# Kernel optimization log

Hardware: AMD Instinct MI355X
Metric: run time of the kernel (lower is better)

## Reference

```python
import jax, jax.numpy as jnp
import numpy as np
from jax import lax

DIM = 96
B, H, W = 4, 256, 256


def setup_inputs() -> dict:
    key = jax.random.key(0)
    ks = jax.random.split(key, 20)
    f = lambda k, s, scale=0.05: (jax.random.normal(k, s, dtype=jnp.float32) * scale)
    d = DIM
    return {
        "x": jax.random.normal(ks[0], (B, d, H, W), dtype=jnp.float32),
        "prompt": jax.random.normal(ks[1], (B, d), dtype=jnp.float32),
        "scale_weights": jax.random.uniform(ks[2], (B, 3), dtype=jnp.float32),
        "ln_w": jnp.ones((d,), jnp.float32),
        "ln_b": jnp.zeros((d,), jnp.float32),
        "e0_pw_w": f(ks[3], (d, d)),       # expert0 pointwise 1x1: [out, in]
        "e0_pw_b": f(ks[4], (d,)),
        "e0_dw_w": f(ks[5], (d, 1, 3, 3)),  # depthwise 3x3
        "e0_dw_b": f(ks[6], (d,)),
        "e1_dw_w": f(ks[7], (d, 1, 3, 3)),  # depthwise 3x3, dilation 2
        "e1_dw_b": f(ks[8], (d,)),
        "e2_dw_w": f(ks[9], (d, 1, 5, 5)),  # depthwise 5x5, dilation 3
        "e2_dw_b": f(ks[10], (d,)),
        "proj_w": f(ks[11], (d, d)),
        "proj_b": f(ks[12], (d,)),
        "ffn1_w": f(ks[13], (2 * d, d)),
        "ffn1_b": f(ks[14], (2 * d,)),
        "ffn2_w": f(ks[15], (d, 2 * d)),
        "ffn2_b": f(ks[16], (d,)),
    }


def _conv1x1(x, w, b):
    # x: [B,C,H,W], w: [O,C]
    return jnp.einsum('bchw,oc->bohw', x, w) + b[None, :, None, None]


def _dwconv(x, w, b, dilation, pad):
    # depthwise conv, w: [C,1,k,k]
    c = x.shape[1]
    y = lax.conv_general_dilated(
        x, w, window_strides=(1, 1),
        padding=[(pad, pad), (pad, pad)],
        rhs_dilation=(dilation, dilation),
        feature_group_count=c,
        dimension_numbers=('NCHW', 'OIHW', 'NCHW'))
    return y + b[None, :, None, None]


def _layernorm_c(x, w, b, eps=1e-6):
    # LayerNorm over channel dim of NCHW (torch permutes to NHWC, norms last dim)
    mu = jnp.mean(x, axis=1, keepdims=True)
    var = jnp.mean((x - mu) ** 2, axis=1, keepdims=True)
    xn = (x - mu) * lax.rsqrt(var + eps)
    return xn * w[None, :, None, None] + b[None, :, None, None]


def reference(x, prompt, scale_weights, ln_w, ln_b,
              e0_pw_w, e0_pw_b, e0_dw_w, e0_dw_b,
              e1_dw_w, e1_dw_b, e2_dw_w, e2_dw_b,
              proj_w, proj_b, ffn1_w, ffn1_b, ffn2_w, ffn2_b):
    shortcut = x
    xn = _layernorm_c(x, ln_w, ln_b)

    # Three receptive-field experts (all run densely, soft-weighted)
    e0 = _dwconv(_conv1x1(xn, e0_pw_w, e0_pw_b), e0_dw_w, e0_dw_b, dilation=1, pad=1)
    e1 = _dwconv(xn, e1_dw_w, e1_dw_b, dilation=2, pad=2)
    e2 = _dwconv(xn, e2_dw_w, e2_dw_b, dilation=3, pad=6)

    w = scale_weights  # [B,3]
    x_adaptive = (w[:, 0, None, None, None] * e0
                  + w[:, 1, None, None, None] * e1
                  + w[:, 2, None, None, None] * e2)
    x_adaptive = x_adaptive * (1.0 + prompt[:, :, None, None])

    x1 = shortcut + _conv1x1(x_adaptive, proj_w, proj_b)
    h = jax.nn.gelu(_conv1x1(x1, ffn1_w, ffn1_b), approximate=False)
    out = x1 + _conv1x1(h, ffn2_w, ffn2_b)
    return out
```

## Files before the change

### kernel.cpp

```cpp
#include <hip/hip_runtime.h>
#include <hip/hip_bf16.h>

typedef __hip_bfloat16 bf16;
typedef __attribute__((ext_vector_type(8))) __bf16 bf16x8;
typedef __attribute__((ext_vector_type(4))) float  f32x4;

#define HW   65536
#define WID  256
#define CC   96
#define NB   4
static const size_t S_ELEMS = (size_t)NB * CC * HW;

__device__ __forceinline__ float lo2f(unsigned u) { unsigned x = u << 16;        return __builtin_bit_cast(float, x); }
__device__ __forceinline__ float hi2f(unsigned u) { unsigned x = u & 0xffff0000u; return __builtin_bit_cast(float, x); }
__device__ __forceinline__ unsigned short f2bu(float f) {
    return __builtin_bit_cast(unsigned short, __float2bfloat16(f));
}

__device__ __forceinline__ float gelu_erf(float v) {
    float z  = fabsf(v) * 0.70710678118654752f;
    float t  = __builtin_amdgcn_rcpf(1.f + 0.3275911f * z);
    float poly = t * (0.254829592f + t * (-0.284496736f + t * (1.421413741f
               + t * (-1.453152027f + t * 1.061405429f))));
    float erfz = 1.f - poly * __expf(-z * z);
    float erfv = copysignf(erfz, v);
    return 0.5f * v * (1.f + erfv);
}

__global__ __launch_bounds__(256) void ln_kernel(
    const float* __restrict__ x, const float* __restrict__ lw,
    const float* __restrict__ lb, bf16* __restrict__ y)
{
    int t  = blockIdx.x * 256 + threadIdx.x;
    int b  = t >> 15;
    int hw = (t & 32767) * 2;
    size_t base = (size_t)b * CC * HW + hw;

    float s0 = 0.f, s1 = 0.f, q0 = 0.f, q1 = 0.f;
    for (int c = 0; c < CC; ++c) {
        float2 v = *reinterpret_cast<const float2*>(&x[base + (size_t)c * HW]);
        s0 += v.x; s1 += v.y; q0 += v.x * v.x; q1 += v.y * v.y;
    }
    float mu0 = s0 * (1.f / 96.f), mu1 = s1 * (1.f / 96.f);
    float rs0 = rsqrtf(q0 * (1.f / 96.f) - mu0 * mu0 + 1e-6f);
    float rs1 = rsqrtf(q1 * (1.f / 96.f) - mu1 * mu1 + 1e-6f);

    for (int c = 0; c < CC; ++c) {
        float2 v = *reinterpret_cast<const float2*>(&x[base + (size_t)c * HW]);
        float g = lw[c], be = lb[c];
        bf16 o[2];
        o[0] = __float2bfloat16((v.x - mu0) * rs0 * g + be);
        o[1] = __float2bfloat16((v.y - mu1) * rs1 * g + be);
        *reinterpret_cast<uint*>(&y[base + (size_t)c * HW]) = *reinterpret_cast<uint*>(o);
    }
}

__device__ __forceinline__ int swzo(int row, int col, int width) {
    return (row * width + col) ^ ((((row & 7) ^ ((row >> 3) & 7)) << 3));
}

template <typename TI, typename TOT, int CIN, int COUT, bool GELU, bool HASRES>
__global__ __launch_bounds__(256) void conv1x1_mfma(
    const TI* __restrict__ in, const float* __restrict__ wgt,
    const float* __restrict__ bias, const float* __restrict__ resid,
    TOT* __restrict__ out)
{
    constexpr int KSPLIT = CIN / 96;
    constexpr int OSPLIT = COUT / 96;
    constexpr int MT     = 6;
    static_assert(CIN == KSPLIT * 96 && COUT == OSPLIT * 96, "96-multiples only");

    __shared__ unsigned short s_w[96 * 96];
    __shared__ unsigned short s_x[128 * 96];
    __shared__ float          s_b[COUT];

    const int tid  = threadIdx.x;
    const int lane = tid & 63;
    const int wave = tid >> 6;
    const int q    = lane >> 4;
    const int n    = lane & 15;

    const int pos0 = blockIdx.x * 128;
    const int b    = pos0 >> 16;
    const int hw0  = pos0 & 65535;

    for (int k = tid; k < COUT; k += 256) s_b[k] = bias[k];

    const TI* inb = in + (size_t)b * CIN * HW;
    const int pl0 = wave * 32 + n;
    const int pl1 = pl0 + 16;

#pragma unroll
    for (int os = 0; os < OSPLIT; ++os) {
        f32x4 acc[MT][2];
#pragma unroll
        for (int mt = 0; mt < MT; ++mt) {
            acc[mt][0] = {0.f, 0.f, 0.f, 0.f};
            acc[mt][1] = {0.f, 0.f, 0.f, 0.f};
        }

#pragma unroll
        for (int ks = 0; ks < KSPLIT; ++ks) {
            for (int k = tid; k < 96 * 24; k += 256) {
                int o = k / 24, c4 = (k - o * 24) * 4;
                float4 w4 = *reinterpret_cast<const float4*>(
                    &wgt[(size_t)(os * 96 + o) * CIN + ks * 96 + c4]);
                ushort4 pk = make_ushort4(f2bu(w4.x), f2bu(w4.y), f2bu(w4.z), f2bu(w4.w));
                *reinterpret_cast<ushort4*>(&s_w[swzo(o, c4, 96)]) = pk;
            }
            if (KSPLIT > 1 || os == 0) {
                for (int idx = tid; idx < 48 * 16; idx += 256) {
                    const int cp = idx >> 4;
                    const int pb = idx & 15;
                    const TI* gp = inb + (size_t)(ks * 96 + 2 * cp) * HW + hw0 + pb * 8;
                    unsigned short ua[8], ub[8];
                    if constexpr (__is_same(TI, float)) {
                        float4 a0 = *reinterpret_cast<const float4*>(gp);
                        float4 a1 = *reinterpret_cast<const float4*>(gp + 4);
                        float4 b0 = *reinterpret_cast<const float4*>(gp + HW);
                        float4 b1 = *reinterpret_cast<const float4*>(gp + HW + 4);
                        ua[0]=f2bu(a0.x); ua[1]=f2bu(a0.y); ua[2]=f2bu(a0.z); ua[3]=f2bu(a0.w);
                        ua[4]=f2bu(a1.x); ua[5]=f2bu(a1.y); ua[6]=f2bu(a1.z); ua[7]=f2bu(a1.w);
                        ub[0]=f2bu(b0.x); ub[1]=f2bu(b0.y); ub[2]=f2bu(b0.z); ub[3]=f2bu(b0.w);
                        ub[4]=f2bu(b1.x); ub[5]=f2bu(b1.y); ub[6]=f2bu(b1.z); ub[7]=f2bu(b1.w);
                    } else {
                        *reinterpret_cast<uint4*>(ua) = *reinterpret_cast<const uint4*>(gp);
                        *reinterpret_cast<uint4*>(ub) = *reinterpret_cast<const uint4*>(gp + HW);
                    }
#pragma unroll
                    for (int i = 0; i < 8; ++i) {
                        uint d = (uint)ua[i] | ((uint)ub[i] << 16);
                        *reinterpret_cast<uint*>(&s_x[swzo(pb * 8 + i, 2 * cp, 96)]) = d;
                    }
                }
            }
            __syncthreads();

#pragma unroll
            for (int kt = 0; kt < 3; ++kt) {
                const int col = kt * 32 + q * 8;
                union { unsigned short u[8]; bf16x8 v; } bf0, bf1;
                *reinterpret_cast<uint4*>(bf0.u) =
                    *reinterpret_cast<const uint4*>(&s_x[swzo(pl0, col, 96)]);
                *reinterpret_cast<uint4*>(bf1.u) =
                    *reinterpret_cast<const uint4*>(&s_x[swzo(pl1, col, 96)]);
#pragma unroll
                for (int mt = 0; mt < MT; ++mt) {
                    union { unsigned short u[8]; bf16x8 v; } fa;
                    *reinterpret_cast<uint4*>(fa.u) =
                        *reinterpret_cast<const uint4*>(&s_w[swzo(mt * 16 + n, col, 96)]);
                    acc[mt][0] = __builtin_amdgcn_mfma_f32_16x16x32_bf16(fa.v, bf0.v, acc[mt][0], 0, 0, 0);
                    acc[mt][1] = __builtin_amdgcn_mfma_f32_16x16x32_bf16(fa.v, bf1.v, acc[mt][1], 0, 0, 0);
                }
            }
            if (os + 1 < OSPLIT || ks + 1 < KSPLIT)
                __syncthreads();
        }

        const int p0 = hw0 + pl0;
        const int p1 = hw0 + pl1;
        const size_t obase = (size_t)b * COUT * HW;
#pragma unroll
        for (int mt = 0; mt < MT; ++mt) {
#pragma unroll
            for (int nt = 0; nt < 2; ++nt) {
                const int p = (nt == 0) ? p0 : p1;
#pragma unroll
                for (int r = 0; r < 4; ++r) {
                    const int o = os * 96 + mt * 16 + q * 4 + r;
                    float v = acc[mt][nt][r] + s_b[o];
                    if constexpr (GELU) v = gelu_erf(v);
                    const size_t idx = obase + (size_t)o * HW + p;
                    if constexpr (HASRES) v += resid[idx];
                    if constexpr (__is_same(TOT, float)) out[idx] = v;
                    else                                 out[idx] = __float2bfloat16(v);
                }
            }
        }
    }
}

__global__ __launch_bounds__(256) void ffn_fused(
    const bf16* __restrict__ xa, const float* __restrict__ x,
    const float* __restrict__ pw, const float* __restrict__ pb,
    const float* __restrict__ w1, const float* __restrict__ b1,
    const float* __restrict__ w2, const float* __restrict__ b2,
    float* __restrict__ out)
{
    constexpr int HP = 104;
    __shared__ unsigned short s_w[96 * 96];
    __shared__ unsigned short s_x1[128 * HP];
    __shared__ unsigned short s_hx[128 * HP];
    __shared__ float          s_bias[384];

    const int tid  = threadIdx.x;
    const int lane = tid & 63;
    const int wave = tid >> 6;
    const int q    = lane >> 4;
    const int n    = lane & 15;

    const int pos0 = blockIdx.x * 128;
    const int b    = pos0 >> 16;
    const int hw0  = pos0 & 65535;
    const int pl0  = wave * 32 + n;
    const int pl1  = pl0 + 16;

    auto stage_w = [&](const float* W, int row0, int col0, int rstride) {
        for (int k = tid; k < 96 * 24; k += 256) {
            int o = k / 24, c4 = (k - o * 24) * 4;
            float4 w4 = *reinterpret_cast<const float4*>(
                &W[(size_t)(row0 + o) * rstride + col0 + c4]);
            ushort4 pk = make_ushort4(f2bu(w4.x), f2bu(w4.y), f2bu(w4.z), f2bu(w4.w));
            *reinterpret_cast<ushort4*>(&s_w[swzo(o, c4, 96)]) = pk;
        }
    };
    auto gemm_swz = [&](f32x4 (&acc)[6][2]) {
#pragma unroll
        for (int kt = 0; kt < 3; ++kt) {
            const int col = kt * 32 + q * 8;
            union { unsigned short u[8]; bf16x8 v; } bf0, bf1;
            *reinterpret_cast<uint4*>(bf0.u) =
                *reinterpret_cast<const uint4*>(&s_hx[swzo(pl0, col, 96)]);
            *reinterpret_cast<uint4*>(bf1.u) =
                *reinterpret_cast<const uint4*>(&s_hx[swzo(pl1, col, 96)]);
#pragma unroll
            for (int mt = 0; mt < 6; ++mt) {
                union { unsigned short u[8]; bf16x8 v; } fa;
                *reinterpret_cast<uint4*>(fa.u) =
                    *reinterpret_cast<const uint4*>(&s_w[swzo(mt * 16 + n, col, 96)]);
                acc[mt][0] = __builtin_amdgcn_mfma_f32_16x16x32_bf16(fa.v, bf0.v, acc[mt][0], 0, 0, 0);
                acc[mt][1] = __builtin_amdgcn_mfma_f32_16x16x32_bf16(fa.v, bf1.v, acc[mt][1], 0, 0, 0);
            }
        }
    };
    auto gemm_lin = [&](const unsigned short* B, f32x4 (&acc)[6][2]) {
#pragma unroll
        for (int kt = 0; kt < 3; ++kt) {
            const int col = kt * 32 + q * 8;
            union { unsigned short u[8]; bf16x8 v; } bf0, bf1;
            *reinterpret_cast<uint4*>(bf0.u) =
                *reinterpret_cast<const uint4*>(&B[pl0 * HP + col]);
            *reinterpret_cast<uint4*>(bf1.u) =
                *reinterpret_cast<const uint4*>(&B[pl1 * HP + col]);
#pragma unroll
            for (int mt = 0; mt < 6; ++mt) {
                union { unsigned short u[8]; bf16x8 v; } fa;
                *reinterpret_cast<uint4*>(fa.u) =
                    *reinterpret_cast<const uint4*>(&s_w[swzo(mt * 16 + n, col, 96)]);
                acc[mt][0] = __builtin_amdgcn_mfma_f32_16x16x32_bf16(fa.v, bf0.v, acc[mt][0], 0, 0, 0);
                acc[mt][1] = __builtin_amdgcn_mfma_f32_16x16x32_bf16(fa.v, bf1.v, acc[mt][1], 0, 0, 0);
            }
        }
    };
    auto st4 = [&](unsigned short* dst, int elem, float v0, float v1, float v2, float v3) {
        union { unsigned short u[4]; uint2 d; } t;
        t.u[0] = f2bu(v0); t.u[1] = f2bu(v1); t.u[2] = f2bu(v2); t.u[3] = f2bu(v3);
        *reinterpret_cast<uint2*>(&dst[elem]) = t.d;
    };

    {
        const bf16* inb = xa + (size_t)b * 96 * HW;
        for (int idx = tid; idx < 48 * 16; idx += 256) {
            const int cp = idx >> 4, pbk = idx & 15;
            const bf16* gp = inb + (size_t)(2 * cp) * HW + hw0 + pbk * 8;
            unsigned short ua[8], ub[8];
            *reinterpret_cast<uint4*>(ua) = *reinterpret_cast<const uint4*>(gp);
            *reinterpret_cast<uint4*>(ub) = *reinterpret_cast<const uint4*>(gp + HW);
#pragma unroll
            for (int i = 0; i < 8; ++i) {
                uint d = (uint)ua[i] | ((uint)ub[i] << 16);
                *reinterpret_cast<uint*>(&s_hx[swzo(pbk * 8 + i, 2 * cp, 96)]) = d;
            }
        }
    }
    stage_w(pw, 0, 0, 96);
    if (tid < 96)  s_bias[tid]       = pb[tid];
    if (tid < 192) s_bias[96 + tid]  = b1[tid];
    if (tid < 96)  s_bias[288 + tid] = b2[tid];
    __syncthreads();

    float xr[6][2][4];
    {
        const size_t xbase = (size_t)b * 96 * HW;
#pragma unroll
        for (int mt = 0; mt < 6; ++mt)
#pragma unroll
            for (int nt = 0; nt < 2; ++nt) {
                const int p = hw0 + (nt ? pl1 : pl0);
#pragma unroll
                for (int r = 0; r < 4; ++r)
                    xr[mt][nt][r] = x[xbase + (size_t)(mt * 16 + q * 4 + r) * HW + p];
            }
    }
    f32x4 accp[6][2];
#pragma unroll
    for (int mt = 0; mt < 6; ++mt) { accp[mt][0] = {0,0,0,0}; accp[mt][1] = {0,0,0,0}; }
    gemm_swz(accp);

    float x1f[6][2][4];
#pragma unroll
    for (int mt = 0; mt < 6; ++mt)
#pragma unroll
        for (int nt = 0; nt < 2; ++nt) {
            const int p = nt ? pl1 : pl0;
#pragma unroll
            for (int r = 0; r < 4; ++r)
                x1f[mt][nt][r] = accp[mt][nt][r] + s_bias[mt * 16 + q * 4 + r] + xr[mt][nt][r];
            st4(s_x1, p * HP + mt * 16 + q * 4,
                x1f[mt][nt][0], x1f[mt][nt][1], x1f[mt][nt][2], x1f[mt][nt][3]);
        }
    __syncthreads();

    stage_w(w1, 0, 0, 96);
    __syncthreads();
    f32x4 acc1[6][2];
#pragma unroll
    for (int mt = 0; mt < 6; ++mt) { acc1[mt][0] = {0,0,0,0}; acc1[mt][1] = {0,0,0,0}; }
    gemm_lin(s_x1, acc1);
#pragma unroll
    for (int mt = 0; mt < 6; ++mt)
#pragma unroll
        for (int nt = 0; nt < 2; ++nt) {
            const int p = nt ? pl1 : pl0;
            float v0 = gelu_erf(acc1[mt][nt][0] + s_bias[96 + mt * 16 + q * 4 + 0]);
            float v1 = gelu_erf(acc1[mt][nt][1] + s_bias[96 + mt * 16 + q * 4 + 1]);
            float v2 = gelu_erf(acc1[mt][nt][2] + s_bias[96 + mt * 16 + q * 4 + 2]);
            float v3 = gelu_erf(acc1[mt][nt][3] + s_bias[96 + mt * 16 + q * 4 + 3]);
            st4(s_hx, p * HP + mt * 16 + q * 4, v0, v1, v2, v3);
        }
    __syncthreads();

    stage_w(w1, 96, 0, 96);
    __syncthreads();
    f32x4 acc1b[6][2];
#pragma unroll
    for (int mt = 0; mt < 6; ++mt) { acc1b[mt][0] = {0,0,0,0}; acc1b[mt][1] = {0,0,0,0}; }
    gemm_lin(s_x1, acc1b);
    __syncthreads();

    stage_w(w2, 0, 0, 192);
    __syncthreads();
    f32x4 acc2[6][2];
#pragma unroll
    for (int mt = 0; mt < 6; ++mt) { acc2[mt][0] = {0,0,0,0}; acc2[mt][1] = {0,0,0,0}; }
    gemm_lin(s_hx, acc2);
    __syncthreads();

    stage_w(w2, 0, 96, 192);
#pragma unroll
    for (int mt = 0; mt < 6; ++mt)
#pragma unroll
        for (int nt = 0; nt < 2; ++nt) {
            const int p = nt ? pl1 : pl0;
            float v0 = gelu_erf(acc1b[mt][nt][0] + s_bias[192 + mt * 16 + q * 4 + 0]);
            float v1 = gelu_erf(acc1b[mt][nt][1] + s_bias[192 + mt * 16 + q * 4 + 1]);
            float v2 = gelu_erf(acc1b[mt][nt][2] + s_bias[192 + mt * 16 + q * 4 + 2]);
            float v3 = gelu_erf(acc1b[mt][nt][3] + s_bias[192 + mt * 16 + q * 4 + 3]);
            st4(s_hx, p * HP + mt * 16 + q * 4, v0, v1, v2, v3);
        }
    __syncthreads();
    gemm_lin(s_hx, acc2);

    const size_t obase = (size_t)b * 96 * HW;
#pragma unroll
    for (int mt = 0; mt < 6; ++mt)
#pragma unroll
        for (int nt = 0; nt < 2; ++nt) {
            const int p = hw0 + (nt ? pl1 : pl0);
#pragma unroll
            for (int r = 0; r < 4; ++r) {
                const int o = mt * 16 + q * 4 + r;
                out[obase + (size_t)o * HW + p] =
                    x1f[mt][nt][r] + acc2[mt][nt][r] + s_bias[288 + o];
            }
        }
}

#define XR     20
#define XPITCH 22
#define TPITCH 10
#define XCOLS  268
#define TCOLS  258

__global__ __launch_bounds__(256) void experts_kernel(
    const bf16* __restrict__ xn, const bf16* __restrict__ t0,
    const float* __restrict__ w0, const float* __restrict__ b0,
    const float* __restrict__ w1, const float* __restrict__ b1,
    const float* __restrict__ w2, const float* __restrict__ b2,
    const float* __restrict__ sw, const float* __restrict__ prompt,
    bf16* __restrict__ xa)
{
    __shared__ alignas(16) unsigned short sxT[XCOLS * XPITCH];
    __shared__ alignas(16) unsigned short stT[TCOLS * TPITCH];

    const int tid  = threadIdx.x;
    const int lane = tid & 63;
    const int wave = tid >> 6;
    const int bid = blockIdx.x;
    const int h0  = (bid & 31) * 8;
    const int bc  = bid >> 5;
    const int b   = bc / 96;
    const int c   = bc - b * 96;
    const size_t pbase = (size_t)bc * HW;

    const bf16* xp = xn + pbase;
    const bf16* tp = t0 + pbase;
    uint* sx32 = reinterpret_cast<uint*>(sxT);
    uint* st32 = reinterpret_cast<uint*>(stT);

    if (tid < 132) {
        int cc = tid / 11, d = tid - cc * 11;
        int col = (cc < 6) ? cc : 256 + cc;
        sx32[col * 11 + d] = 0u;
    } else if (tid < 142) {
        int i = tid - 132;
        int col = (i < 5) ? 0 : 257;
        int d   = (i < 5) ? i : i - 5;
        st32[col * 5 + d] = 0u;
    }

    {
        const int rp = (lane >> 2) & 7;
        const int ch = 8 * wave + (lane & 3) + ((lane >> 5) << 2);
        const int gh0 = h0 - 6 + 2 * rp, gh1 = gh0 + 1;
        union { uint4 q; unsigned short u[8]; } a, bb;
        a.q  = ((unsigned)gh0 < 256u) ? *reinterpret_cast<const uint4*>(xp + gh0 * WID + ch * 8)
                                      : make_uint4(0u, 0u, 0u, 0u);
        bb.q = ((unsigned)gh1 < 256u) ? *reinterpret_cast<const uint4*>(xp + gh1 * WID + ch * 8)
                                      : make_uint4(0u, 0u, 0u, 0u);
        const int base = 11 * (6 + 8 * ch) + rp;
#pragma unroll
        for (int j = 0; j < 8; ++j)
            sx32[base + 11 * j] = (uint)a.u[j] | ((uint)bb.u[j] << 16);
    }
    if (wave == 2) {
        const int rp = 8 + ((lane >> 2) & 1);
        const int ch = (lane & 3) + (((lane >> 3) & 7) << 2);
        const int gh0 = h0 - 6 + 2 * rp, gh1 = gh0 + 1;
        union { uint4 q; unsigned short u[8]; } a, bb;
        a.q  = ((unsigned)gh0 < 256u) ? *reinterpret_cast<const uint4*>(xp + gh0 * WID + ch * 8)
                                      : make_uint4(0u, 0u, 0u, 0u);
        bb.q = ((unsigned)gh1 < 256u) ? *reinterpret_cast<const uint4*>(xp + gh1 * WID + ch * 8)
                                      : make_uint4(0u, 0u, 0u, 0u);
        const int base = 11 * (6 + 8 * ch) + rp;
#pragma unroll
        for (int j = 0; j < 8; ++j)
            sx32[base + 11 * j] = (uint)a.u[j] | ((uint)bb.u[j] << 16);
    }
    if (wave < 2) {
        const int rp = (lane >> 3) & 3;
        const int ch = 16 * wave + (lane & 7) + ((lane >> 5) << 3);
        const int gh0 = h0 - 1 + 2 * rp, gh1 = gh0 + 1;
        union { uint4 q; unsigned short u[8]; } a, bb;
        a.q  = ((unsigned)gh0 < 256u) ? *reinterpret_cast<const uint4*>(tp + gh0 * WID + ch * 8)
                                      : make_uint4(0u, 0u, 0u, 0u);
        bb.q = ((unsigned)gh1 < 256u) ? *reinterpret_cast<const uint4*>(tp + gh1 * WID + ch * 8)
                                      : make_uint4(0u, 0u, 0u, 0u);
        const int base = 5 * (1 + 8 * ch) + rp;
#pragma unroll
        for (int j = 0; j < 8; ++j)
            st32[base + 5 * j] = (uint)a.u[j] | ((uint)bb.u[j] << 16);
    }
    if (wave == 3 && lane < 32) {
        const int rp = 4;
        const int ch = lane;
        const int gh0 = h0 - 1 + 2 * rp, gh1 = gh0 + 1;
        union { uint4 q; unsigned short u[8]; } a, bb;
        a.q  = ((unsigned)gh0 < 256u) ? *reinterpret_cast<const uint4*>(tp + gh0 * WID + ch * 8)
                                      : make_uint4(0u, 0u, 0u, 0u);
        bb.q = ((unsigned)gh1 < 256u) ? *reinterpret_cast<const uint4*>(tp + gh1 * WID + ch * 8)
                                      : make_uint4(0u, 0u, 0u, 0u);
        const int base = 5 * (1 + 8 * ch) + rp;
#pragma unroll
        for (int j = 0; j < 8; ++j)
            st32[base + 5 * j] = (uint)a.u[j] | ((uint)bb.u[j] << 16);
    }

    float wk0[9], wk1[9], wk2[25];
#pragma unroll
    for (int i = 0; i < 9; ++i)  wk0[i] = w0[c * 9 + i];
#pragma unroll
    for (int i = 0; i < 9; ++i)  wk1[i] = w1[c * 9 + i];
#pragma unroll
    for (int i = 0; i < 25; ++i) wk2[i] = w2[c * 25 + i];
    const float bb0 = b0[c], bb1 = b1[c], bb2 = b2[c];
    const float s0 = sw[b * 3 + 0], s1 = sw[b * 3 + 1], s2 = sw[b * 3 + 2];
    const float pr = 1.f + prompt[b * 96 + c];

    __syncthreads();

    const int w = tid;
    float acc0[8], acc1[8], acc2[8];
#pragma unroll
    for (int r = 0; r < 8; ++r) { acc0[r] = bb0; acc1[r] = bb1; acc2[r] = bb2; }

    const unsigned short* bx = &sxT[w * XPITCH];
    const unsigned short* bt = &stT[w * TPITCH];

#pragma unroll
    for (int kw = 0; kw < 5; ++kw) {
        float cv[20];
#pragma unroll
        for (int j = 0; j < 10; ++j) {
            unsigned u = *reinterpret_cast<const unsigned*>(&bx[kw * 3 * XPITCH + 2 * j]);
            cv[2 * j]     = lo2f(u);
            cv[2 * j + 1] = hi2f(u);
        }
#pragma unroll
        for (int kh = 0; kh < 5; ++kh) {
            const float wv = wk2[kh * 5 + kw];
#pragma unroll
            for (int r = 0; r < 8; ++r) acc2[r] += wv * cv[r + 3 * kh];
        }
        if (kw == 2) {
#pragma unroll
            for (int kh = 0; kh < 3; ++kh) {
                const float wv = wk1[kh * 3 + 1];
#pragma unroll
                for (int r = 0; r < 8; ++r) acc1[r] += wv * cv[r + 2 * kh + 4];
            }
        }
    }
#pragma unroll
    for (int kwh = 0; kwh < 2; ++kwh) {
        const int kw = kwh * 2;
        float cv[12];
#pragma unroll
        for (int j = 0; j < 6; ++j) {
            unsigned u = *reinterpret_cast<const unsigned*>(&bx[(4 + 2 * kw) * XPITCH + 4 + 2 * j]);
            cv[2 * j]     = lo2f(u);
            cv[2 * j + 1] = hi2f(u);
        }
#pragma unroll
        for (int kh = 0; kh < 3; ++kh) {
            const float wv = wk1[kh * 3 + kw];
#pragma unroll
            for (int r = 0; r < 8; ++r) acc1[r] += wv * cv[r + 2 * kh];
        }
    }
#pragma unroll
    for (int kw = 0; kw < 3; ++kw) {
        float cv[10];
#pragma unroll
        for (int j = 0; j < 5; ++j) {
            unsigned u = *reinterpret_cast<const unsigned*>(&bt[kw * TPITCH + 2 * j]);
            cv[2 * j]     = lo2f(u);
            cv[2 * j + 1] = hi2f(u);
        }
#pragma unroll
        for (int kh = 0; kh < 3; ++kh) {
            const float wv = wk0[kh * 3 + kw];
#pragma unroll
            for (int r = 0; r < 8; ++r) acc0[r] += wv * cv[r + kh];
        }
    }

    bf16* op = xa + pbase + (size_t)h0 * WID + w;
#pragma unroll
    for (int r = 0; r < 8; ++r) {
        float v = (s0 * acc0[r] + s1 * acc1[r] + s2 * acc2[r]) * pr;
        op[r * WID] = __float2bfloat16(v);
    }
}

extern "C" void kernel_launch(void* const* d_in, const int* in_sizes, int n_in,
                              void* d_out, int out_size, void* d_ws, size_t ws_size,
                              hipStream_t stream)
{
    const float* x       = (const float*)d_in[0];
    const float* prompt  = (const float*)d_in[1];
    const float* sw      = (const float*)d_in[2];
    const float* ln_w    = (const float*)d_in[3];
    const float* ln_b    = (const float*)d_in[4];
    const float* e0_pw_w = (const float*)d_in[5];
    const float* e0_pw_b = (const float*)d_in[6];
    const float* e0_dw_w = (const float*)d_in[7];
    const float* e0_dw_b = (const float*)d_in[8];
    const float* e1_dw_w = (const float*)d_in[9];
    const float* e1_dw_b = (const float*)d_in[10];
    const float* e2_dw_w = (const float*)d_in[11];
    const float* e2_dw_b = (const float*)d_in[12];
    const float* proj_w  = (const float*)d_in[13];
    const float* proj_b  = (const float*)d_in[14];
    const float* ffn1_w  = (const float*)d_in[15];
    const float* ffn1_b  = (const float*)d_in[16];
    const float* ffn2_w  = (const float*)d_in[17];
    const float* ffn2_b  = (const float*)d_in[18];

    float* out = (float*)d_out;
    bf16*  ws  = (bf16*)d_ws;
    bf16*  A   = ws;
    bf16*  Bt  = ws + S_ELEMS;
    bf16*  Cx  = ws + 2 * S_ELEMS;

    ln_kernel<<<512, 256, 0, stream>>>(x, ln_w, ln_b, A);
    conv1x1_mfma<bf16, bf16, 96, 96, false, false>
        <<<2048, 256, 0, stream>>>(A, e0_pw_w, e0_pw_b, nullptr, Bt);
    experts_kernel<<<12288, 256, 0, stream>>>(A, Bt, e0_dw_w, e0_dw_b, e1_dw_w, e1_dw_b,
                                              e2_dw_w, e2_dw_b, sw, prompt, Cx);
    ffn_fused<<<2048, 256, 0, stream>>>(Cx, x, proj_w, proj_b,
                                        ffn1_w, ffn1_b, ffn2_w, ffn2_b, out);
}
```

Measured before the change: 495.4 us.

## Restructure FFN kernel to 512 threads with register-prefetched weight staging

The fused proj/FFN kernel now runs 8 waves per block, each handling 16 positions instead of 32, which halves per-thread accumulator and residual register arrays. Weight tiles for the next GEMM are prefetched into registers (WLOAD) while the current GEMM runs and written to shared memory afterwards (WWRITE), hiding global weight-load latency. The x1/hidden buffers switch from padded linear layout to the swizzled layout used elsewhere. The cost is less MFMA reuse of each A fragment per wave and more barrier participants per block.

After: 491.9 us. No clear change (-0.7%).

```diff
diff --git a/kernel.cpp b/kernel.cpp
--- a/kernel.cpp
+++ b/kernel.cpp
@@ -180,87 +180,79 @@
     }
 }
 
-__global__ __launch_bounds__(256) void ffn_fused(
+__global__ __launch_bounds__(512, 4) void ffn_fused(
     const bf16* __restrict__ xa, const float* __restrict__ x,
     const float* __restrict__ pw, const float* __restrict__ pb,
     const float* __restrict__ w1, const float* __restrict__ b1,
     const float* __restrict__ w2, const float* __restrict__ b2,
     float* __restrict__ out)
 {
-    constexpr int HP = 104;
     __shared__ unsigned short s_w[96 * 96];
-    __shared__ unsigned short s_x1[128 * HP];
-    __shared__ unsigned short s_hx[128 * HP];
+    __shared__ unsigned short s_x1[128 * 96];
+    __shared__ unsigned short s_hx[128 * 96];
     __shared__ float          s_bias[384];
 
     const int tid  = threadIdx.x;
     const int lane = tid & 63;
-    const int wave = tid >> 6;
+    const int w8   = tid >> 6;
     const int q    = lane >> 4;
     const int n    = lane & 15;
 
     const int pos0 = blockIdx.x * 128;
     const int b    = pos0 >> 16;
     const int hw0  = pos0 & 65535;
-    const int pl0  = wave * 32 + n;
-    const int pl1  = pl0 + 16;
-
-    auto stage_w = [&](const float* W, int row0, int col0, int rstride) {
-        for (int k = tid; k < 96 * 24; k += 256) {
-            int o = k / 24, c4 = (k - o * 24) * 4;
-            float4 w4 = *reinterpret_cast<const float4*>(
-                &W[(size_t)(row0 + o) * rstride + col0 + c4]);
-            ushort4 pk = make_ushort4(f2bu(w4.x), f2bu(w4.y), f2bu(w4.z), f2bu(w4.w));
-            *reinterpret_cast<ushort4*>(&s_w[swzo(o, c4, 96)]) = pk;
+    const int pl   = w8 * 16 + n;
+    const int p    = hw0 + pl;
+
+    float4 wr[5];
+    auto WLOAD = [&](const float* W, int row0, int col0, int rs) {
+#pragma unroll
+        for (int i = 0; i < 5; ++i) {
+            const int idx = tid + i * 512;
+            if (i < 4 || tid < 256) {
+                const int o = idx / 24, c4 = (idx - o * 24) * 4;
+                wr[i] = *reinterpret_cast<const float4*>(
+                    &W[(size_t)(row0 + o) * rs + col0 + c4]);
+            }
         }
     };
-    auto gemm_swz = [&](f32x4 (&acc)[6][2]) {
+    auto WWRITE = [&]() {
+#pragma unroll
+        for (int i = 0; i < 5; ++i) {
+            const int idx = tid + i * 512;
+            if (i < 4 || tid < 256) {
+                const int o = idx / 24, c4 = (idx - o * 24) * 4;
+                ushort4 pk = make_ushort4(f2bu(wr[i].x), f2bu(wr[i].y),
+                                          f2bu(wr[i].z), f2bu(wr[i].w));
+                *reinterpret_cast<ushort4*>(&s_w[swzo(o, c4, 96)]) = pk;
+            }
+        }
+    };
+    auto GEMM = [&](const unsigned short* B, f32x4 (&acc)[6]) {
 #pragma unroll
         for (int kt = 0; kt < 3; ++kt) {
             const int col = kt * 32 + q * 8;
-            union { unsigned short u[8]; bf16x8 v; } bf0, bf1;
-            *reinterpret_cast<uint4*>(bf0.u) =
-                *reinterpret_cast<const uint4*>(&s_hx[swzo(pl0, col, 96)]);
-            *reinterpret_cast<uint4*>(bf1.u) =
-                *reinterpret_cast<const uint4*>(&s_hx[swzo(pl1, col, 96)]);
+            union { unsigned short u[8]; bf16x8 v; } bf;
+            *reinterpret_cast<uint4*>(bf.u) =
+                *reinterpret_cast<const uint4*>(&B[swzo(pl, col, 96)]);
 #pragma unroll
             for (int mt = 0; mt < 6; ++mt) {
                 union { unsigned short u[8]; bf16x8 v; } fa;
                 *reinterpret_cast<uint4*>(fa.u) =
                     *reinterpret_cast<const uint4*>(&s_w[swzo(mt * 16 + n, col, 96)]);
-                acc[mt][0] = __builtin_amdgcn_mfma_f32_16x16x32_bf16(fa.v, bf0.v, acc[mt][0], 0, 0, 0);
-                acc[mt][1] = __builtin_amdgcn_mfma_f32_16x16x32_bf16(fa.v, bf1.v, acc[mt][1], 0, 0, 0);
+                acc[mt] = __builtin_amdgcn_mfma_f32_16x16x32_bf16(fa.v, bf.v, acc[mt], 0, 0, 0);
             }
         }
     };
-    auto gemm_lin = [&](const unsigned short* B, f32x4 (&acc)[6][2]) {
-#pragma unroll
-        for (int kt = 0; kt < 3; ++kt) {
-            const int col = kt * 32 + q * 8;
-            union { unsigned short u[8]; bf16x8 v; } bf0, bf1;
-            *reinterpret_cast<uint4*>(bf0.u) =
-                *reinterpret_cast<const uint4*>(&B[pl0 * HP + col]);
-            *reinterpret_cast<uint4*>(bf1.u) =
-                *reinterpret_cast<const uint4*>(&B[pl1 * HP + col]);
-#pragma unroll
-            for (int mt = 0; mt < 6; ++mt) {
-                union { unsigned short u[8]; bf16x8 v; } fa;
-                *reinterpret_cast<uint4*>(fa.u) =
-                    *reinterpret_cast<const uint4*>(&s_w[swzo(mt * 16 + n, col, 96)]);
-                acc[mt][0] = __builtin_amdgcn_mfma_f32_16x16x32_bf16(fa.v, bf0.v, acc[mt][0], 0, 0, 0);
-                acc[mt][1] = __builtin_amdgcn_mfma_f32_16x16x32_bf16(fa.v, bf1.v, acc[mt][1], 0, 0, 0);
-            }
-        }
-    };
-    auto st4 = [&](unsigned short* dst, int elem, float v0, float v1, float v2, float v3) {
+    auto ST4 = [&](unsigned short* dst, int col4, float v0, float v1, float v2, float v3) {
         union { unsigned short u[4]; uint2 d; } t;
         t.u[0] = f2bu(v0); t.u[1] = f2bu(v1); t.u[2] = f2bu(v2); t.u[3] = f2bu(v3);
-        *reinterpret_cast<uint2*>(&dst[elem]) = t.d;
+        *reinterpret_cast<uint2*>(&dst[swzo(pl, col4, 96)]) = t.d;
     };
 
     {
         const bf16* inb = xa + (size_t)b * 96 * HW;
-        for (int idx = tid; idx < 48 * 16; idx += 256) {
+        for (int idx = tid; idx < 48 * 16; idx += 512) {
             const int cp = idx >> 4, pbk = idx & 15;
             const bf16* gp = inb + (size_t)(2 * cp) * HW + hw0 + pbk * 8;
             unsigned short ua[8], ub[8];
@@ -272,108 +264,108 @@
                 *reinterpret_cast<uint*>(&s_hx[swzo(pbk * 8 + i, 2 * cp, 96)]) = d;
             }
         }
-    }
-    stage_w(pw, 0, 0, 96);
-    if (tid < 96)  s_bias[tid]       = pb[tid];
-    if (tid < 192) s_bias[96 + tid]  = b1[tid];
-    if (tid < 96)  s_bias[288 + tid] = b2[tid];
-    __syncthreads();
-
-    float xr[6][2][4];
+        for (int k = tid; k < 96 * 24; k += 512) {
+            const int o = k / 24, c4 = (k - o * 24) * 4;
+            float4 w4 = *reinterpret_cast<const float4*>(&pw[(size_t)o * 96 + c4]);
+            ushort4 pk = make_ushort4(f2bu(w4.x), f2bu(w4.y), f2bu(w4.z), f2bu(w4.w));
+            *reinterpret_cast<ushort4*>(&s_w[swzo(o, c4, 96)]) = pk;
+        }
+        if (tid < 96)  s_bias[tid]       = pb[tid];
+        if (tid < 192) s_bias[96 + tid]  = b1[tid];
+        if (tid < 96)  s_bias[288 + tid] = b2[tid];
+    }
+    __syncthreads();
+
+    WLOAD(w1, 0, 0, 96);
+    float xr[6][4];
     {
         const size_t xbase = (size_t)b * 96 * HW;
 #pragma unroll
         for (int mt = 0; mt < 6; ++mt)
 #pragma unroll
-            for (int nt = 0; nt < 2; ++nt) {
-                const int p = hw0 + (nt ? pl1 : pl0);
-#pragma unroll
-                for (int r = 0; r < 4; ++r)
-                    xr[mt][nt][r] = x[xbase + (size_t)(mt * 16 + q * 4 + r) * HW + p];
-            }
-    }
-    f32x4 accp[6][2];
-#pragma unroll
-    for (int mt = 0; mt < 6; ++mt) { accp[mt][0] = {0,0,0,0}; accp[mt][1] = {0,0,0,0}; }
-    gemm_swz(accp);
-
-    float x1f[6][2][4];
-#pragma unroll
-    for (int mt = 0; mt < 6; ++mt)
-#pragma unroll
-        for (int nt = 0; nt < 2; ++nt) {
-            const int p = nt ? pl1 : pl0;
-#pragma unroll
             for (int r = 0; r < 4; ++r)
-                x1f[mt][nt][r] = accp[mt][nt][r] + s_bias[mt * 16 + q * 4 + r] + xr[mt][nt][r];
-            st4(s_x1, p * HP + mt * 16 + q * 4,
-                x1f[mt][nt][0], x1f[mt][nt][1], x1f[mt][nt][2], x1f[mt][nt][3]);
-        }
-    __syncthreads();
-
-    stage_w(w1, 0, 0, 96);
-    __syncthreads();
-    f32x4 acc1[6][2];
-#pragma unroll
-    for (int mt = 0; mt < 6; ++mt) { acc1[mt][0] = {0,0,0,0}; acc1[mt][1] = {0,0,0,0}; }
-    gemm_lin(s_x1, acc1);
-#pragma unroll
-    for (int mt = 0; mt < 6; ++mt)
-#pragma unroll
-        for (int nt = 0; nt < 2; ++nt) {
-            const int p = nt ? pl1 : pl0;
-            float v0 = gelu_erf(acc1[mt][nt][0] + s_bias[96 + mt * 16 + q * 4 + 0]);
-            float v1 = gelu_erf(acc1[mt][nt][1] + s_bias[96 + mt * 16 + q * 4 + 1]);
-            float v2 = gelu_erf(acc1[mt][nt][2] + s_bias[96 + mt * 16 + q * 4 + 2]);
-            float v3 = gelu_erf(acc1[mt][nt][3] + s_bias[96 + mt * 16 + q * 4 + 3]);
-            st4(s_hx, p * HP + mt * 16 + q * 4, v0, v1, v2, v3);
-        }
-    __syncthreads();
-
-    stage_w(w1, 96, 0, 96);
-    __syncthreads();
-    f32x4 acc1b[6][2];
-#pragma unroll
-    for (int mt = 0; mt < 6; ++mt) { acc1b[mt][0] = {0,0,0,0}; acc1b[mt][1] = {0,0,0,0}; }
-    gemm_lin(s_x1, acc1b);
-    __syncthreads();
-
-    stage_w(w2, 0, 0, 192);
-    __syncthreads();
-    f32x4 acc2[6][2];
-#pragma unroll
-    for (int mt = 0; mt < 6; ++mt) { acc2[mt][0] = {0,0,0,0}; acc2[mt][1] = {0,0,0,0}; }
-    gemm_lin(s_hx, acc2);
-    __syncthreads();
-
-    stage_w(w2, 0, 96, 192);
-#pragma unroll
-    for (int mt = 0; mt < 6; ++mt)
-#pragma unroll
-        for (int nt = 0; nt < 2; ++nt) {
-            const int p = nt ? pl1 : pl0;
-            float v0 = gelu_erf(acc1b[mt][nt][0] + s_bias[192 + mt * 16 + q * 4 + 0]);
-            float v1 = gelu_erf(acc1b[mt][nt][1] + s_bias[192 + mt * 16 + q * 4 + 1]);
-            float v2 = gelu_erf(acc1b[mt][nt][2] + s_bias[192 + mt * 16 + q * 4 + 2]);
-            float v3 = gelu_erf(acc1b[mt][nt][3] + s_bias[192 + mt * 16 + q * 4 + 3]);
-            st4(s_hx, p * HP + mt * 16 + q * 4, v0, v1, v2, v3);
-        }
-    __syncthreads();
-    gemm_lin(s_hx, acc2);
-
-    const size_t obase = (size_t)b * 96 * HW;
-#pragma unroll
-    for (int mt = 0; mt < 6; ++mt)
-#pragma unroll
-        for (int nt = 0; nt < 2; ++nt) {
-            const int p = hw0 + (nt ? pl1 : pl0);
+                xr[mt][r] = x[xbase + (size_t)(mt * 16 + q * 4 + r) * HW + p];
+    }
+    float x1f[6][4];
+    {
+        f32x4 accp[6];
+#pragma unroll
+        for (int mt = 0; mt < 6; ++mt) accp[mt] = {0.f, 0.f, 0.f, 0.f};
+        GEMM(s_hx, accp);
+#pragma unroll
+        for (int mt = 0; mt < 6; ++mt) {
+#pragma unroll
+            for (int r = 0; r < 4; ++r)
+                x1f[mt][r] = accp[mt][r] + s_bias[mt * 16 + q * 4 + r] + xr[mt][r];
+            ST4(s_x1, mt * 16 + q * 4, x1f[mt][0], x1f[mt][1], x1f[mt][2], x1f[mt][3]);
+        }
+    }
+    __syncthreads();
+
+    WWRITE();
+    __syncthreads();
+
+    WLOAD(w2, 0, 0, 192);
+    {
+        f32x4 a1[6];
+#pragma unroll
+        for (int mt = 0; mt < 6; ++mt) a1[mt] = {0.f, 0.f, 0.f, 0.f};
+        GEMM(s_x1, a1);
+#pragma unroll
+        for (int mt = 0; mt < 6; ++mt) {
+            float v0 = gelu_erf(a1[mt][0] + s_bias[96 + mt * 16 + q * 4 + 0]);
+            float v1 = gelu_erf(a1[mt][1] + s_bias[96 + mt * 16 + q * 4 + 1]);
+            float v2 = gelu_erf(a1[mt][2] + s_bias[96 + mt * 16 + q * 4 + 2]);
+            float v3 = gelu_erf(a1[mt][3] + s_bias[96 + mt * 16 + q * 4 + 3]);
+            ST4(s_hx, mt * 16 + q * 4, v0, v1, v2, v3);
+        }
+    }
+    __syncthreads();
+
+    WWRITE();
+    __syncthreads();
+
+    f32x4 acc2[6];
+#pragma unroll
+    for (int mt = 0; mt < 6; ++mt) acc2[mt] = {0.f, 0.f, 0.f, 0.f};
+    WLOAD(w1, 96, 0, 96);
+    GEMM(s_hx, acc2);
+    __syncthreads();
+
+    WWRITE();
+    __syncthreads();
+
+    WLOAD(w2, 0, 96, 192);
+    {
+        f32x4 a1[6];
+#pragma unroll
+        for (int mt = 0; mt < 6; ++mt) a1[mt] = {0.f, 0.f, 0.f, 0.f};
+        GEMM(s_x1, a1);
+#pragma unroll
+        for (int mt = 0; mt < 6; ++mt) {
+            float v0 = gelu_erf(a1[mt][0] + s_bias[192 + mt * 16 + q * 4 + 0]);
+            float v1 = gelu_erf(a1[mt][1] + s_bias[192 + mt * 16 + q * 4 + 1]);
+            float v2 = gelu_erf(a1[mt][2] + s_bias[192 + mt * 16 + q * 4 + 2]);
+            float v3 = gelu_erf(a1[mt][3] + s_bias[192 + mt * 16 + q * 4 + 3]);
+            ST4(s_hx, mt * 16 + q * 4, v0, v1, v2, v3);
+        }
+    }
+    __syncthreads();
+
+    WWRITE();
+    __syncthreads();
+
+    GEMM(s_hx, acc2);
+    {
+        const size_t obase = (size_t)b * 96 * HW;
+#pragma unroll
+        for (int mt = 0; mt < 6; ++mt)
 #pragma unroll
             for (int r = 0; r < 4; ++r) {
                 const int o = mt * 16 + q * 4 + r;
-                out[obase + (size_t)o * HW + p] =
-                    x1f[mt][nt][r] + acc2[mt][nt][r] + s_bias[288 + o];
-            }
-        }
+                out[obase + (size_t)o * HW + p] = x1f[mt][r] + acc2[mt][r] + s_bias[288 + o];
+            }
+    }
 }
 
 #define XR     20
@@ -598,6 +590,6 @@
         <<<2048, 256, 0, stream>>>(A, e0_pw_w, e0_pw_b, nullptr, Bt);
     experts_kernel<<<12288, 256, 0, stream>>>(A, Bt, e0_dw_w, e0_dw_b, e1_dw_w, e1_dw_b,
                                               e2_dw_w, e2_dw_b, sw, prompt, Cx);
-    ffn_fused<<<2048, 256, 0, stream>>>(Cx, x, proj_w, proj_b,
+    ffn_fused<<<2048, 512, 0, stream>>>(Cx, x, proj_w, proj_b,
                                         ffn1_w, ffn1_b, ffn2_w, ffn2_b, out);
 }
```
